# Kernel optimization log

Measured on AMD Instinct MI355X. Metric: run time of the kernel, lower is better.

## Reference

```python
import jax, jax.numpy as jnp
import numpy as np
import math

HIDDEN = 1024
HEADS = 16
HEAD_DIM = HIDDEN // HEADS
B, S = 4, 2048


def setup_inputs() -> dict:
    key = jax.random.key(0)
    ks = jax.random.split(key, 10)
    scale = 1.0 / math.sqrt(HIDDEN)
    inp = {
        "x": jax.random.normal(ks[0], (B, S, HIDDEN), dtype=jnp.float32),
        "attention_mask": jnp.ones((B, 1, 1, S), dtype=jnp.int32),
        "Wq": jax.random.normal(ks[1], (HIDDEN, HIDDEN), dtype=jnp.float32) * scale,
        "bq": jnp.zeros((HIDDEN,), dtype=jnp.float32),
        "Wk": jax.random.normal(ks[2], (HIDDEN, HIDDEN), dtype=jnp.float32) * scale,
        "bk": jnp.zeros((HIDDEN,), dtype=jnp.float32),
        "Wv": jax.random.normal(ks[3], (HIDDEN, HIDDEN), dtype=jnp.float32) * scale,
        "bv": jnp.zeros((HIDDEN,), dtype=jnp.float32),
        "Wo": jax.random.normal(ks[4], (HIDDEN, HIDDEN), dtype=jnp.float32) * scale,
        "bo": jnp.zeros((HIDDEN,), dtype=jnp.float32),
    }
    return inp


def reference(x, attention_mask, Wq, bq, Wk, bk, Wv, bv, Wo, bo):
    b, s, d = x.shape
    # nn.Linear: x @ W.T + b
    q = (x @ Wq.T + bq).reshape(b, s, HEADS, HEAD_DIM).transpose(0, 2, 1, 3)
    k = (x @ Wk.T + bk).reshape(b, s, HEADS, HEAD_DIM).transpose(0, 2, 1, 3)
    v = (x @ Wv.T + bv).reshape(b, s, HEADS, HEAD_DIM).transpose(0, 2, 1, 3)
    # explicit O(S^2) score matrix, as in the original
    scores = jnp.einsum("bhqd,bhkd->bhqk", q, k) / math.sqrt(HEAD_DIM)
    scores = jnp.where(attention_mask == 0, jnp.float32(-1e9), scores)
    attn = jax.nn.softmax(scores, axis=-1)
    # dropout(p=0.1) treated as identity (eval mode) for a deterministic reference
    out = jnp.einsum("bhqk,bhkd->bhqd", attn, v)
    out = out.transpose(0, 2, 1, 3).reshape(b, s, d)
    return out @ Wo.T + bo
```

## Files before the change

kernel.cpp:

```cpp
#include <hip/hip_runtime.h>
#include <math.h>

#define HID 1024
#define NH  16
#define HD  64
#define NB  4
#define SL  2048
#define MROWS (NB * SL)

typedef __attribute__((ext_vector_type(8))) short short8;
typedef __attribute__((ext_vector_type(4))) float f32x4;
typedef unsigned short ushort_t;
typedef unsigned int uint_t;

__device__ __forceinline__ uint_t f2bf(float x) {
    union { float f; uint_t u; } a; a.f = x;
    return (a.u + 0x7fffu + ((a.u >> 16) & 1u)) >> 16;
}

__device__ __forceinline__ void load_lds16(const void* g, void* l) {
    __builtin_amdgcn_global_load_lds(
        (const __attribute__((address_space(1))) void*)g,
        (__attribute__((address_space(3))) void*)l, 16, 0, 0);
}

__device__ __forceinline__ void gemm_core_bk64(
    const ushort_t* __restrict__ A, const ushort_t* __restrict__ B,
    const int m0, const int n0, ushort_t* As, ushort_t* Bs, f32x4 (&acc)[4][4])
{
    const int tid = threadIdx.x;
    const int w = tid >> 6, lane = tid & 63;
    const int wm = (w & 1) << 6, wn = (w >> 1) << 6;
    const int c = lane & 15, quad = lane >> 4;

    for (int k0 = 0; k0 < HID; k0 += 64) {
        __syncthreads();
        #pragma unroll
        for (int rd = 0; rd < 4; ++rd) {
            const int g = rd * 4 + w;
            const int idx = g * 64 + lane;
            const int r = idx >> 3, sc = idx & 7;
            const int dc = sc ^ (r & 7);
            load_lds16(&A[(size_t)(m0 + r) * HID + k0 + dc * 8], As + g * 512);
            load_lds16(&B[(size_t)(n0 + r) * HID + k0 + dc * 8], Bs + g * 512);
        }
        __syncthreads();

        #pragma unroll
        for (int ks = 0; ks < 2; ++ks) {
            short8 af[4], bf[4];
            #pragma unroll
            for (int i = 0; i < 4; ++i) {
                const int ra = wm + i * 16 + c;
                const int rb = wn + i * 16 + c;
                af[i] = *(const short8*)
                    &As[ra * 64 + ((((ks << 2) + quad) ^ (c & 7)) << 3)];
                bf[i] = *(const short8*)
                    &Bs[rb * 64 + ((((ks << 2) + quad) ^ (c & 7)) << 3)];
            }
            #pragma unroll
            for (int i = 0; i < 4; ++i)
                #pragma unroll
                for (int j = 0; j < 4; ++j)
                    acc[i][j] = __builtin_amdgcn_mfma_f32_16x16x32_bf16(
                        af[i], bf[j], acc[i][j], 0, 0, 0);
        }
    }
}

__global__ __launch_bounds__(256) void cvt_bf16_kernel(
    const float* __restrict__ x,
    const float* __restrict__ wq, const float* __restrict__ wk,
    const float* __restrict__ wv, const float* __restrict__ wo,
    ushort_t* __restrict__ xb, ushort_t* __restrict__ wqb,
    ushort_t* __restrict__ wkb, ushort_t* __restrict__ wvb,
    ushort_t* __restrict__ wob)
{
    const int seg = blockIdx.y;
    const float* src; ushort_t* dst;
    if (seg < 8)       { src = x + (size_t)seg * 1048576; dst = xb + (size_t)seg * 1048576; }
    else if (seg == 8) { src = wq; dst = wqb; }
    else if (seg == 9) { src = wk; dst = wkb; }
    else if (seg == 10){ src = wv; dst = wvb; }
    else               { src = wo; dst = wob; }
    const int i = (blockIdx.x * 256 + threadIdx.x) * 8;
    const float4 a = *(const float4*)&src[i];
    const float4 b = *(const float4*)&src[i + 4];
    uint4 o;
    o.x = f2bf(a.x) | (f2bf(a.y) << 16);
    o.y = f2bf(a.z) | (f2bf(a.w) << 16);
    o.z = f2bf(b.x) | (f2bf(b.y) << 16);
    o.w = f2bf(b.z) | (f2bf(b.w) << 16);
    *(uint4*)&dst[i] = o;
}

__global__ __launch_bounds__(256) void qkv_mfma_kernel(
    const ushort_t* __restrict__ xb,
    const ushort_t* __restrict__ wqb, const ushort_t* __restrict__ wkb,
    const ushort_t* __restrict__ wvb,
    const float* __restrict__ bq, const float* __restrict__ bk,
    const float* __restrict__ bv,
    ushort_t* __restrict__ qo, ushort_t* __restrict__ ko,
    ushort_t* __restrict__ vo)
{
    __shared__ __align__(16) ushort_t As[128 * 64];
    __shared__ __align__(16) ushort_t Bs[128 * 64];

    const int wsel = blockIdx.z;
    const ushort_t* W    = (wsel == 0) ? wqb : (wsel == 1) ? wkb : wvb;
    const float*    bias = (wsel == 0) ? bq  : (wsel == 1) ? bk  : bv;

    const int flat = blockIdx.x + (blockIdx.y << 3);
    const int xcd = flat & 7, s = flat >> 3;
    const int m0 = ((xcd << 3) + (s >> 3)) * 128;
    const int n0 = (s & 7) * 128;

    f32x4 acc[4][4];
    const f32x4 zero = {0.f, 0.f, 0.f, 0.f};
    #pragma unroll
    for (int i = 0; i < 4; ++i)
        #pragma unroll
        for (int j = 0; j < 4; ++j) acc[i][j] = zero;

    gemm_core_bk64(xb, W, m0, n0, As, Bs, acc);

    const int tid = threadIdx.x;
    const int w = tid >> 6, lane = tid & 63;
    const int wm = (w & 1) << 6, wn = (w >> 1) << 6;
    const int c = lane & 15, quad = lane >> 4;
    const float qscale = (wsel == 0) ? 0.18033688f : 1.0f;

    #pragma unroll
    for (int j = 0; j < 4; ++j) {
        const int n_g = n0 + wn + j * 16 + c;
        const float bj = bias[n_g];
        const int h = n_g >> 6, d = n_g & 63;
        #pragma unroll
        for (int i = 0; i < 4; ++i) {
            const int mbase = m0 + wm + i * 16 + quad * 4;
            const int b = mbase >> 11;
            const int sbase = mbase & (SL - 1);
            if (wsel == 2) {
                ushort4 pk;
                pk.x = (ushort_t)f2bf(acc[i][j][0] + bj);
                pk.y = (ushort_t)f2bf(acc[i][j][1] + bj);
                pk.z = (ushort_t)f2bf(acc[i][j][2] + bj);
                pk.w = (ushort_t)f2bf(acc[i][j][3] + bj);
                *(ushort4*)&vo[(((size_t)(b * NH + h) * HD) + d) * SL + sbase] = pk;
            } else {
                ushort_t* dst = (wsel == 0) ? qo : ko;
                #pragma unroll
                for (int reg = 0; reg < 4; ++reg) {
                    const float v = (acc[i][j][reg] + bj) * qscale;
                    dst[(((size_t)(b * NH + h) * SL) + sbase + reg) * HD + d] =
                        (ushort_t)f2bf(v);
                }
            }
        }
    }
}

__global__ __launch_bounds__(256, 4) void attn_mfma_kernel(
    const ushort_t* __restrict__ q, const ushort_t* __restrict__ k,
    const ushort_t* __restrict__ vt, const int* __restrict__ mask,
    ushort_t* __restrict__ ao)
{
    __shared__ __align__(16) ushort_t Ks[64 * 64];
    __shared__ __align__(16) ushort_t Vs[64 * 64];
    __shared__ __align__(16) ushort_t Ps[128 * 64];

    const int qt = blockIdx.x;
    const int bh = blockIdx.y;
    const int b = bh >> 4, h = bh & 15;
    const int tid = threadIdx.x;
    const int w = tid >> 6, lane = tid & 63;
    const int c = lane & 15, quad = lane >> 4;

    const ushort_t* qp = q  + (size_t)bh * SL * HD + (size_t)qt * 128 * HD;
    const ushort_t* kp = k  + (size_t)bh * SL * HD;
    const ushort_t* vp = vt + (size_t)bh * HD * SL;

    short8 qf[2][2];
    #pragma unroll
    for (int mi = 0; mi < 2; ++mi)
        #pragma unroll
        for (int ks = 0; ks < 2; ++ks)
            qf[mi][ks] = *(const short8*)&qp[(size_t)(w * 32 + mi * 16 + c) * HD
                                             + ks * 32 + quad * 8];

    int kfo[4][2], vfo[4][2], pfo[2][2], pwo[2][4];
    #pragma unroll
    for (int ni = 0; ni < 4; ++ni)
        #pragma unroll
        for (int ks = 0; ks < 2; ++ks) {
            kfo[ni][ks] = (4 * c + ni) * 64 + (((ks * 4 + quad) ^ (c & 7)) << 3);
            vfo[ni][ks] = (ni * 16 + c) * 64 + (((ks * 4 + quad) ^ (c & 7)) << 3);
        }
    #pragma unroll
    for (int mi = 0; mi < 2; ++mi) {
        #pragma unroll
        for (int ks = 0; ks < 2; ++ks) {
            const int prow = w * 32 + mi * 16 + c;
            pfo[mi][ks] = prow * 64 + (((ks * 4 + quad) ^ (prow & 7)) << 3);
        }
        #pragma unroll
        for (int reg = 0; reg < 4; ++reg) {
            const int prow = w * 32 + mi * 16 + quad * 4 + reg;
            pwo[mi][reg] = prow * 64 + (((c >> 1) ^ (prow & 7)) * 8)
                           + ((c & 1) * 4);
        }
    }

    const ushort_t* kst[2]; const ushort_t* vst[2];
    #pragma unroll
    for (int rd = 0; rd < 2; ++rd) {
        const int t = (rd * 4 + w) * 64 + lane;
        const int r = t >> 3, sc = t & 7;
        kst[rd] = kp + (size_t)r * HD + (sc ^ ((r >> 2) & 7)) * 8;
        vst[rd] = vp + (size_t)r * SL + (sc ^ (r & 7)) * 8;
    }
    const int* mp = mask + b * SL + 4 * c;

    float l_s[2][4] = {};
    f32x4 oa[2][4];
    const f32x4 zero = {0.f, 0.f, 0.f, 0.f};
    #pragma unroll
    for (int mi = 0; mi < 2; ++mi)
        #pragma unroll
        for (int ni = 0; ni < 4; ++ni) oa[mi][ni] = zero;

    for (int kt = 0; kt < SL / 64; ++kt) {
        __syncthreads();
        load_lds16(kst[0], Ks + (0 * 4 + w) * 512);
        load_lds16(vst[0], Vs + (0 * 4 + w) * 512);
        load_lds16(kst[1], Ks + (1 * 4 + w) * 512);
        load_lds16(vst[1], Vs + (1 * 4 + w) * 512);
        kst[0] += 64 * HD; kst[1] += 64 * HD;
        vst[0] += 64;      vst[1] += 64;
        __syncthreads();

        f32x4 sf[2][4];
        #pragma unroll
        for (int mi = 0; mi < 2; ++mi)
            #pragma unroll
            for (int ni = 0; ni < 4; ++ni) sf[mi][ni] = zero;
        #pragma unroll
        for (int ni = 0; ni < 4; ++ni) {
            #pragma unroll
            for (int ks = 0; ks < 2; ++ks) {
                const short8 kf = *(const short8*)&Ks[kfo[ni][ks]];
                #pragma unroll
                for (int mi = 0; mi < 2; ++mi)
                    sf[mi][ni] = __builtin_amdgcn_mfma_f32_16x16x32_bf16(
                        qf[mi][ks], kf, sf[mi][ni], 0, 0, 0);
            }
        }

        const int4 mzv = *(const int4*)mp;
        mp += 64;
        const int mz[4] = {mzv.x, mzv.y, mzv.z, mzv.w};

        #pragma unroll
        for (int mi = 0; mi < 2; ++mi) {
            #pragma unroll
            for (int reg = 0; reg < 4; ++reg) {
                float p[4];
                #pragma unroll
                for (int ni = 0; ni < 4; ++ni) {
                    float pv = __builtin_amdgcn_exp2f(sf[mi][ni][reg]);
                    p[ni] = (mz[ni] == 0) ? 0.f : pv;
                }
                l_s[mi][reg] += (p[0] + p[1]) + (p[2] + p[3]);
                union { float f; uint_t u; } u0, u1, u2, u3;
                u0.f = p[0]; u1.f = p[1]; u2.f = p[2]; u3.f = p[3];
                uint2 pk;
                pk.x = __builtin_amdgcn_perm(u1.u, u0.u, 0x07060302u);
                pk.y = __builtin_amdgcn_perm(u3.u, u2.u, 0x07060302u);
                *(uint2*)&Ps[pwo[mi][reg]] = pk;
            }
        }

        short8 pf[2][2];
        #pragma unroll
        for (int mi = 0; mi < 2; ++mi)
            #pragma unroll
            for (int ks = 0; ks < 2; ++ks)
                pf[mi][ks] = *(const short8*)&Ps[pfo[mi][ks]];
        #pragma unroll
        for (int ni = 0; ni < 4; ++ni) {
            #pragma unroll
            for (int ks = 0; ks < 2; ++ks) {
                const short8 vf = *(const short8*)&Vs[vfo[ni][ks]];
                #pragma unroll
                for (int mi = 0; mi < 2; ++mi)
                    oa[mi][ni] = __builtin_amdgcn_mfma_f32_16x16x32_bf16(
                        pf[mi][ks], vf, oa[mi][ni], 0, 0, 0);
            }
        }
    }

    #pragma unroll
    for (int mi = 0; mi < 2; ++mi) {
        #pragma unroll
        for (int reg = 0; reg < 4; ++reg) {
            float l = l_s[mi][reg];
            #pragma unroll
            for (int off = 1; off < 16; off <<= 1)
                l += __shfl_xor(l, off, 64);
            const float inv = 1.f / l;
            const int s_g = qt * 128 + w * 32 + mi * 16 + quad * 4 + reg;
            #pragma unroll
            for (int ni = 0; ni < 4; ++ni) {
                const int d = ni * 16 + c;
                ao[((size_t)(b * SL + s_g)) * HID + h * HD + d] =
                    (ushort_t)f2bf(oa[mi][ni][reg] * inv);
            }
        }
    }
}

__global__ __launch_bounds__(256) void out_mfma_kernel(
    const ushort_t* __restrict__ aob, const ushort_t* __restrict__ wob,
    const float* __restrict__ bo, float* __restrict__ out)
{
    __shared__ __align__(16) ushort_t As[128 * 64];
    __shared__ __align__(16) ushort_t Bs[128 * 64];

    const int flat = blockIdx.x + (blockIdx.y << 3);
    const int xcd = flat & 7, s = flat >> 3;
    const int m0 = ((xcd << 3) + (s >> 3)) * 128;
    const int n0 = (s & 7) * 128;

    f32x4 acc[4][4];
    const f32x4 zero = {0.f, 0.f, 0.f, 0.f};
    #pragma unroll
    for (int i = 0; i < 4; ++i)
        #pragma unroll
        for (int j = 0; j < 4; ++j) acc[i][j] = zero;

    gemm_core_bk64(aob, wob, m0, n0, As, Bs, acc);

    const int tid = threadIdx.x;
    const int w = tid >> 6, lane = tid & 63;
    const int wm = (w & 1) << 6, wn = (w >> 1) << 6;
    const int c = lane & 15, quad = lane >> 4;

    #pragma unroll
    for (int j = 0; j < 4; ++j) {
        const int n_g = n0 + wn + j * 16 + c;
        const float bj = bo[n_g];
        #pragma unroll
        for (int i = 0; i < 4; ++i) {
            const int mbase = m0 + wm + i * 16 + quad * 4;
            #pragma unroll
            for (int reg = 0; reg < 4; ++reg)
                out[(size_t)(mbase + reg) * HID + n_g] = acc[i][j][reg] + bj;
        }
    }
}

extern "C" void kernel_launch(void* const* d_in, const int* in_sizes, int n_in,
                              void* d_out, int out_size, void* d_ws, size_t ws_size,
                              hipStream_t stream)
{
    const float* x    = (const float*)d_in[0];
    const int*   mask = (const int*)d_in[1];
    const float* Wq   = (const float*)d_in[2];
    const float* bq   = (const float*)d_in[3];
    const float* Wk   = (const float*)d_in[4];
    const float* bk   = (const float*)d_in[5];
    const float* Wv   = (const float*)d_in[6];
    const float* bv   = (const float*)d_in[7];
    const float* Wo   = (const float*)d_in[8];
    const float* bo   = (const float*)d_in[9];
    float* out = (float*)d_out;

    ushort_t* p = (ushort_t*)d_ws;
    ushort_t* xb  = p; p += (size_t)MROWS * HID;
    ushort_t* wqb = p; p += (size_t)HID * HID;
    ushort_t* wkb = p; p += (size_t)HID * HID;
    ushort_t* wvb = p; p += (size_t)HID * HID;
    ushort_t* wob = p; p += (size_t)HID * HID;
    ushort_t* qb  = p; p += (size_t)MROWS * HID;
    ushort_t* kb  = p; p += (size_t)MROWS * HID;
    ushort_t* vtb = p; p += (size_t)MROWS * HID;
    ushort_t* aob = p; p += (size_t)MROWS * HID;

    cvt_bf16_kernel<<<dim3(512, 12), 256, 0, stream>>>(
        x, Wq, Wk, Wv, Wo, xb, wqb, wkb, wvb, wob);
    qkv_mfma_kernel<<<dim3(8, 64, 3), 256, 0, stream>>>(
        xb, wqb, wkb, wvb, bq, bk, bv, qb, kb, vtb);
    attn_mfma_kernel<<<dim3(16, 64), 256, 0, stream>>>(
        qb, kb, vtb, mask, aob);
    out_mfma_kernel<<<dim3(8, 64), 256, 0, stream>>>(
        aob, wob, bo, out);
}
```

Before: 286.5 us.

## Double-buffer K/V tiles in LDS and prefetch next tile during compute

The attention kernel now keeps two LDS buffers for the K and V tiles. It issues the async global-to-LDS loads for the next tile before computing on the current one, so there is one barrier per iteration instead of two. The P staging buffer is cut to 16 rows per wave, and the softmax-write, read-back and PV MFMA steps now run once per mi sub-tile in turn. This trades extra LDS (roughly 40KB per block instead of 32KB) for hiding global load latency, at the cost of shorter MFMA chains per P fragment.

```diff
diff --git a/kernel.cpp b/kernel.cpp
--- a/kernel.cpp
+++ b/kernel.cpp
@@ -165,9 +165,9 @@
     const ushort_t* __restrict__ vt, const int* __restrict__ mask,
     ushort_t* __restrict__ ao)
 {
-    __shared__ __align__(16) ushort_t Ks[64 * 64];
-    __shared__ __align__(16) ushort_t Vs[64 * 64];
-    __shared__ __align__(16) ushort_t Ps[128 * 64];
+    __shared__ __align__(16) ushort_t Ks[2][64 * 64];
+    __shared__ __align__(16) ushort_t Vs[2][64 * 64];
+    __shared__ __align__(16) ushort_t Ps[64 * 64];
 
     const int qt = blockIdx.x;
     const int bh = blockIdx.y;
@@ -188,7 +188,7 @@
             qf[mi][ks] = *(const short8*)&qp[(size_t)(w * 32 + mi * 16 + c) * HD
                                              + ks * 32 + quad * 8];
 
-    int kfo[4][2], vfo[4][2], pfo[2][2], pwo[2][4];
+    int kfo[4][2], vfo[4][2], pfo[2], pwo[4];
     #pragma unroll
     for (int ni = 0; ni < 4; ++ni)
         #pragma unroll
@@ -197,18 +197,12 @@
             vfo[ni][ks] = (ni * 16 + c) * 64 + (((ks * 4 + quad) ^ (c & 7)) << 3);
         }
     #pragma unroll
-    for (int mi = 0; mi < 2; ++mi) {
-        #pragma unroll
-        for (int ks = 0; ks < 2; ++ks) {
-            const int prow = w * 32 + mi * 16 + c;
-            pfo[mi][ks] = prow * 64 + (((ks * 4 + quad) ^ (prow & 7)) << 3);
-        }
-        #pragma unroll
-        for (int reg = 0; reg < 4; ++reg) {
-            const int prow = w * 32 + mi * 16 + quad * 4 + reg;
-            pwo[mi][reg] = prow * 64 + (((c >> 1) ^ (prow & 7)) * 8)
-                           + ((c & 1) * 4);
-        }
+    for (int ks = 0; ks < 2; ++ks)
+        pfo[ks] = (w * 16 + c) * 64 + (((ks * 4 + quad) ^ (c & 7)) << 3);
+    #pragma unroll
+    for (int reg = 0; reg < 4; ++reg) {
+        const int prow = w * 16 + quad * 4 + reg;
+        pwo[reg] = prow * 64 + (((c >> 1) ^ (prow & 7)) * 8) + ((c & 1) * 4);
     }
 
     const ushort_t* kst[2]; const ushort_t* vst[2];
@@ -221,6 +215,13 @@
     }
     const int* mp = mask + b * SL + 4 * c;
 
+    load_lds16(kst[0], Ks[0] + (0 * 4 + w) * 512);
+    load_lds16(vst[0], Vs[0] + (0 * 4 + w) * 512);
+    load_lds16(kst[1], Ks[0] + (1 * 4 + w) * 512);
+    load_lds16(vst[1], Vs[0] + (1 * 4 + w) * 512);
+    kst[0] += 64 * HD; kst[1] += 64 * HD;
+    vst[0] += 64;      vst[1] += 64;
+
     float l_s[2][4] = {};
     f32x4 oa[2][4];
     const f32x4 zero = {0.f, 0.f, 0.f, 0.f};
@@ -229,72 +230,75 @@
         #pragma unroll
         for (int ni = 0; ni < 4; ++ni) oa[mi][ni] = zero;
 
-    for (int kt = 0; kt < SL / 64; ++kt) {
-        __syncthreads();
-        load_lds16(kst[0], Ks + (0 * 4 + w) * 512);
-        load_lds16(vst[0], Vs + (0 * 4 + w) * 512);
-        load_lds16(kst[1], Ks + (1 * 4 + w) * 512);
-        load_lds16(vst[1], Vs + (1 * 4 + w) * 512);
-        kst[0] += 64 * HD; kst[1] += 64 * HD;
-        vst[0] += 64;      vst[1] += 64;
-        __syncthreads();
-
-        f32x4 sf[2][4];
-        #pragma unroll
-        for (int mi = 0; mi < 2; ++mi)
-            #pragma unroll
-            for (int ni = 0; ni < 4; ++ni) sf[mi][ni] = zero;
-        #pragma unroll
-        for (int ni = 0; ni < 4; ++ni) {
-            #pragma unroll
-            for (int ks = 0; ks < 2; ++ks) {
-                const short8 kf = *(const short8*)&Ks[kfo[ni][ks]];
-                #pragma unroll
-                for (int mi = 0; mi < 2; ++mi)
-                    sf[mi][ni] = __builtin_amdgcn_mfma_f32_16x16x32_bf16(
-                        qf[mi][ks], kf, sf[mi][ni], 0, 0, 0);
-            }
-        }
-
-        const int4 mzv = *(const int4*)mp;
-        mp += 64;
-        const int mz[4] = {mzv.x, mzv.y, mzv.z, mzv.w};
-
-        #pragma unroll
-        for (int mi = 0; mi < 2; ++mi) {
-            #pragma unroll
-            for (int reg = 0; reg < 4; ++reg) {
-                float p[4];
+    for (int kt0 = 0; kt0 < SL / 64; kt0 += 2) {
+        #pragma unroll
+        for (int half = 0; half < 2; ++half) {
+            const int kt = kt0 + half;
+            const int cur = half, nxt = half ^ 1;
+
+            __syncthreads();
+
+            if (kt + 1 < SL / 64) {
+                load_lds16(kst[0], Ks[nxt] + (0 * 4 + w) * 512);
+                load_lds16(vst[0], Vs[nxt] + (0 * 4 + w) * 512);
+                load_lds16(kst[1], Ks[nxt] + (1 * 4 + w) * 512);
+                load_lds16(vst[1], Vs[nxt] + (1 * 4 + w) * 512);
+            }
+            kst[0] += 64 * HD; kst[1] += 64 * HD;
+            vst[0] += 64;      vst[1] += 64;
+
+            f32x4 sf[2][4];
+            #pragma unroll
+            for (int mi = 0; mi < 2; ++mi)
+                #pragma unroll
+                for (int ni = 0; ni < 4; ++ni) sf[mi][ni] = zero;
+            #pragma unroll
+            for (int ni = 0; ni < 4; ++ni) {
+                #pragma unroll
+                for (int ks = 0; ks < 2; ++ks) {
+                    const short8 kf = *(const short8*)&Ks[cur][kfo[ni][ks]];
+                    #pragma unroll
+                    for (int mi = 0; mi < 2; ++mi)
+                        sf[mi][ni] = __builtin_amdgcn_mfma_f32_16x16x32_bf16(
+                            qf[mi][ks], kf, sf[mi][ni], 0, 0, 0);
+                }
+            }
+
+            const int4 mzv = *(const int4*)mp;
+            mp += 64;
+            const int mz[4] = {mzv.x, mzv.y, mzv.z, mzv.w};
+
+            #pragma unroll
+            for (int mi = 0; mi < 2; ++mi) {
+                #pragma unroll
+                for (int reg = 0; reg < 4; ++reg) {
+                    float p[4];
+                    #pragma unroll
+                    for (int ni = 0; ni < 4; ++ni) {
+                        float pv = __builtin_amdgcn_exp2f(sf[mi][ni][reg]);
+                        p[ni] = (mz[ni] == 0) ? 0.f : pv;
+                    }
+                    l_s[mi][reg] += (p[0] + p[1]) + (p[2] + p[3]);
+                    union { float f; uint_t u; } u0, u1, u2, u3;
+                    u0.f = p[0]; u1.f = p[1]; u2.f = p[2]; u3.f = p[3];
+                    uint2 pk;
+                    pk.x = __builtin_amdgcn_perm(u1.u, u0.u, 0x07060302u);
+                    pk.y = __builtin_amdgcn_perm(u3.u, u2.u, 0x07060302u);
+                    *(uint2*)&Ps[pwo[reg]] = pk;
+                }
+                short8 pf[2];
+                #pragma unroll
+                for (int ks = 0; ks < 2; ++ks)
+                    pf[ks] = *(const short8*)&Ps[pfo[ks]];
                 #pragma unroll
                 for (int ni = 0; ni < 4; ++ni) {
-                    float pv = __builtin_amdgcn_exp2f(sf[mi][ni][reg]);
-                    p[ni] = (mz[ni] == 0) ? 0.f : pv;
+                    #pragma unroll
+                    for (int ks = 0; ks < 2; ++ks) {
+                        const short8 vf = *(const short8*)&Vs[cur][vfo[ni][ks]];
+                        oa[mi][ni] = __builtin_amdgcn_mfma_f32_16x16x32_bf16(
+                            pf[ks], vf, oa[mi][ni], 0, 0, 0);
+                    }
                 }
-                l_s[mi][reg] += (p[0] + p[1]) + (p[2] + p[3]);
-                union { float f; uint_t u; } u0, u1, u2, u3;
-                u0.f = p[0]; u1.f = p[1]; u2.f = p[2]; u3.f = p[3];
-                uint2 pk;
-                pk.x = __builtin_amdgcn_perm(u1.u, u0.u, 0x07060302u);
-                pk.y = __builtin_amdgcn_perm(u3.u, u2.u, 0x07060302u);
-                *(uint2*)&Ps[pwo[mi][reg]] = pk;
-            }
-        }
-
-        short8 pf[2][2];
-        #pragma unroll
-        for (int mi = 0; mi < 2; ++mi)
-            #pragma unroll
-            for (int ks = 0; ks < 2; ++ks)
-                pf[mi][ks] = *(const short8*)&Ps[pfo[mi][ks]];
-        #pragma unroll
-        for (int ni = 0; ni < 4; ++ni) {
-            #pragma unroll
-            for (int ks = 0; ks < 2; ++ks) {
-                const short8 vf = *(const short8*)&Vs[vfo[ni][ks]];
-                #pragma unroll
-                for (int mi = 0; mi < 2; ++mi)
-                    oa[mi][ni] = __builtin_amdgcn_mfma_f32_16x16x32_bf16(
-                        pf[mi][ks], vf, oa[mi][ni], 0, 0, 0);
             }
         }
     }
```

Result: slower. 305.9 us (+6.8%).
